# Kernel optimization log

Measured on AMD Instinct MI355X. Metric: run time of the kernel, lower is better.

Reference implementation:

```python
import jax, jax.numpy as jnp
import numpy as np

# irreps '32x0e + 32x1o + 16x2e': dims 32 (l=0), 96 (l=1, 32x3), 80 (l=2, 16x5) -> 208
MUL0, MUL1, MUL2 = 32, 32, 16
SC = 64  # scalar_channels
N_NODES, N_EDGES = 50000, 200000
FAN_IN = MUL0 * MUL0 + MUL1 * MUL1 + MUL2 * MUL2  # fully-connected path fan-in


def setup_inputs() -> dict:
    key = jax.random.key(0)
    ks = jax.random.split(key, 10)
    node_tensors = jax.random.normal(ks[0], (N_NODES, 208), dtype=jnp.float32)
    edge_index = jax.random.randint(ks[1], (2, N_EDGES), 0, N_NODES)
    # FullyConnectedTensorProduct path weights (mul1, mul2, mul_out)
    W0 = jax.random.normal(ks[2], (MUL0, MUL0, SC), dtype=jnp.float32)
    W1 = jax.random.normal(ks[3], (MUL1, MUL1, SC), dtype=jnp.float32)
    W2 = jax.random.normal(ks[4], (MUL2, MUL2, SC), dtype=jnp.float32)
    # MLP: Linear(64,32) -> SiLU -> Linear(32,1)
    A1 = jax.random.normal(ks[5], (SC, SC // 2), dtype=jnp.float32) / np.float32(np.sqrt(SC))
    b1 = jnp.zeros((SC // 2,), dtype=jnp.float32)
    A2 = jax.random.normal(ks[6], (SC // 2, 1), dtype=jnp.float32) / np.float32(np.sqrt(SC // 2))
    b2 = jnp.zeros((1,), dtype=jnp.float32)
    return {"node_tensors": node_tensors, "edge_index": edge_index,
            "W0": W0, "W1": W1, "W2": W2, "A1": A1, "b1": b1, "A2": A2, "b2": b2}


def _split_irreps(x):
    # x: [E, 208] -> scalars [E,32], vectors [E,32,3], rank-2 [E,16,5]
    s = x[:, :MUL0]
    v = x[:, MUL0:MUL0 + MUL1 * 3].reshape(-1, MUL1, 3)
    t = x[:, MUL0 + MUL1 * 3:].reshape(-1, MUL2, 5)
    return s, v, t


def reference(node_tensors, edge_index, W0, W1, W2, A1, b1, A2, b2):
    src, dst = edge_index[0], edge_index[1]
    x1 = node_tensors[src]  # [E, 208]
    x2 = node_tensors[dst]
    s1, v1, t1 = _split_irreps(x1)
    s2, v2, t2 = _split_irreps(x2)
    alpha = np.float32(1.0 / np.sqrt(FAN_IN))  # path normalization
    # l x l -> 0 Clebsch-Gordan: delta_{m1 m2} / sqrt(2l+1)
    e = alpha * (
        jnp.einsum('eu,ev,uvw->ew', s1, s2, W0)
        + jnp.einsum('eum,evm,uvw->ew', v1, v2, W1) / np.float32(np.sqrt(3.0))
        + jnp.einsum('eum,evm,uvw->ew', t1, t2, W2) / np.float32(np.sqrt(5.0))
    )  # [E, 64]
    h = jax.nn.silu(e @ A1 + b1)
    return (h @ A2 + b2)[:, 0]  # [E]
```

## Files before the change

### kernel.cpp

```cpp
#include <hip/hip_runtime.h>
#include <hip/hip_fp16.h>
#include <stdint.h>

#define N_EDGES 200000
#define N_NODES 50000
#define BM 256
#define NT 512

typedef _Float16 f16x8 __attribute__((ext_vector_type(8)));
typedef float f32x4 __attribute__((ext_vector_type(4)));

__global__ void prep_w(const float* __restrict__ W0, const float* __restrict__ W1,
                       const float* __restrict__ W2, uint16_t* __restrict__ wt) {
  int o = blockIdx.x * 256 + threadIdx.x;
  int T = o >> 11, r = o & 2047, w = r >> 5, kk = r & 31;
  int k = T * 32 + kk;
  const float AS = 1.0f / 48.0f;
  const float AV = AS * 0.57735026918962576f;
  const float AT = AS * 0.44721359549995794f;
  float val;
  if (k < 1024)      val = AS * W0[(k >> 5) * 2048 + (k & 31) * 64 + w];
  else if (k < 2048) { int k2 = k - 1024; val = AV * W1[(k2 >> 5) * 2048 + (k2 & 31) * 64 + w]; }
  else               { int k2 = k - 2048; val = AT * W2[(k2 >> 4) * 1024 + (k2 & 15) * 64 + w]; }
  __half h = __float2half(val);
  wt[o] = *reinterpret_cast<uint16_t*>(&h);
}

__global__ void prep_tables(const float* __restrict__ nt,
                            uint16_t* __restrict__ ta, uint16_t* __restrict__ tb) {
  long long o = (long long)blockIdx.x * 256 + threadIdx.x;
  if (o >= (long long)N_NODES * 296) return;
  int node = (int)(o / 296);
  int r = (int)(o - (long long)node * 296);
  const float* x = nt + (size_t)node * 208;
  float va = 0.f;
  if (r < 32) va = x[r];
  else if (r < 160) { int q = r - 32;  int u = q >> 2, m = q & 3;  if (m < 3) va = x[32 + u * 3 + m]; }
  else if (r < 288) { int q = r - 160; int u = q >> 3, m = q & 7;  if (m < 5) va = x[128 + u * 5 + m]; }
  __half ha = __float2half(va);
  ta[(size_t)node * 296 + r] = *reinterpret_cast<uint16_t*>(&ha);
  if (r < 216) {
    float vb = 0.f;
    if (r < 32) vb = x[r];
    else if (r < 128) { int q = r - 32;  int m = q >> 5, v = q & 31; vb = x[32 + v * 3 + m]; }
    else if (r < 208) { int q = r - 128; int m = q >> 4, v = q & 15; vb = x[128 + v * 5 + m]; }
    __half hb = __float2half(vb);
    tb[(size_t)node * 216 + r] = *reinterpret_cast<uint16_t*>(&hb);
  }
}

__device__ __forceinline__ void gload16(const void* g, void* l) {
  __builtin_amdgcn_global_load_lds(
      (const __attribute__((address_space(1))) void*)g,
      (__attribute__((address_space(3))) void*)l, 16, 0, 0);
}

#define LOADW(WRA, TEXPR)                                                       \
  { int Tc_ = (TEXPR);                                                          \
    _Pragma("unroll") for (int nf = 0; nf < 4; ++nf)                            \
      WRA[nf] = wtg4[Tc_ * 256 + nf * 64 + lo4]; }

#define MSTEP4(WRA, A)                                                          \
  _Pragma("unroll") for (int mf = 0; mf < 4; ++mf)                              \
  _Pragma("unroll") for (int nf = 0; nf < 4; ++nf)                              \
    acc[mf][nf] = __builtin_amdgcn_mfma_f32_16x16x32_f16(                       \
        (A)[mf], *(const f16x8*)&WRA[nf], acc[mf][nf], 0, 0, 0);

#define MSTEP2(WRA, A, H)                                                       \
  _Pragma("unroll") for (int mm = 0; mm < 2; ++mm)                              \
  _Pragma("unroll") for (int nf = 0; nf < 4; ++nf)                              \
    acc[2 * (H) + mm][nf] = __builtin_amdgcn_mfma_f32_16x16x32_f16(             \
        (A)[mm], *(const f16x8*)&WRA[nf], acc[2 * (H) + mm][nf], 0, 0, 0);

#define BUILD_S(T_, A)                                                          \
  _Pragma("unroll") for (int mf = 0; mf < 4; ++mf) {                            \
    __half s1v = *(const __half*)(x1b[mf] + 2 * (T_));                          \
    __half2 s1b2 = __half2half2(s1v);                                           \
    union { uint32_t u[4]; f16x8 v; } au_;                                      \
    _Pragma("unroll") for (int q = 0; q < 4; ++q) {                             \
      __half2 p = __hmul2(s1b2, ((const __half2*)&s2pk[mf])[q]);                \
      au_.u[q] = *(uint32_t*)&p;                                                \
    }                                                                           \
    (A)[mf] = au_.v;                                                            \
  }

#define BUILD_V(U_, A)                                                          \
  _Pragma("unroll") for (int mf = 0; mf < 4; ++mf) {                            \
    uint2 vv_ = *(const uint2*)(x1b[mf] + 64 + (U_) * 8);                       \
    __half2 h01_ = *(__half2*)&vv_.x;                                           \
    __half2 h2x_ = *(__half2*)&vv_.y;                                           \
    __half2 va0 = __half2half2(__low2half(h01_));                               \
    __half2 va1 = __half2half2(__high2half(h01_));                              \
    __half2 va2 = __half2half2(__low2half(h2x_));                               \
    union { uint32_t u[4]; f16x8 v; } au_;                                      \
    _Pragma("unroll") for (int q = 0; q < 4; ++q) {                             \
      __half2 p = __hmul2(va0, ((const __half2*)&v2pk[mf][0])[q]);              \
      p = __hfma2(va1, ((const __half2*)&v2pk[mf][1])[q], p);                   \
      p = __hfma2(va2, ((const __half2*)&v2pk[mf][2])[q], p);                   \
      au_.u[q] = *(uint32_t*)&p;                                                \
    }                                                                           \
    (A)[mf] = au_.v;                                                            \
  }

#define BUILD_TH(TT_, H, A)                                                     \
  _Pragma("unroll") for (int mm = 0; mm < 2; ++mm) {                            \
    int u_ = (TT_) * 2 + (g >> 1);                                              \
    uint4 tv_ = *(const uint4*)(x1b[2 * (H) + mm] + 320 + u_ * 16);             \
    __half2 w01_ = *(__half2*)&tv_.x;                                           \
    __half2 w23_ = *(__half2*)&tv_.y;                                           \
    __half2 w4x_ = *(__half2*)&tv_.z;                                           \
    __half2 tb0 = __half2half2(__low2half(w01_));                               \
    __half2 tb1 = __half2half2(__high2half(w01_));                              \
    __half2 tb2 = __half2half2(__low2half(w23_));                               \
    __half2 tb3 = __half2half2(__high2half(w23_));                              \
    __half2 tb4 = __half2half2(__low2half(w4x_));                               \
    union { uint32_t u[4]; f16x8 v; } au_;                                      \
    _Pragma("unroll") for (int q = 0; q < 4; ++q) {                             \
      __half2 p = __hmul2(tb0, ((const __half2*)&t2pk[mm][0])[q]);              \
      p = __hfma2(tb1, ((const __half2*)&t2pk[mm][1])[q], p);                   \
      p = __hfma2(tb2, ((const __half2*)&t2pk[mm][2])[q], p);                   \
      p = __hfma2(tb3, ((const __half2*)&t2pk[mm][3])[q], p);                   \
      p = __hfma2(tb4, ((const __half2*)&t2pk[mm][4])[q], p);                   \
      au_.u[q] = *(uint32_t*)&p;                                                \
    }                                                                           \
    (A)[mm] = au_.v;                                                            \
  }

#define RING_S(WRA, P, T0) { f16x8 a[4]; BUILD_S((T0) + (P), a); MSTEP4(WRA, a); LOADW(WRA, (T0) + (P) + 4); }
#define RING_V(WRA, P, T0) { f16x8 a[4]; BUILD_V((T0) + (P) - 32, a); MSTEP4(WRA, a); LOADW(WRA, (T0) + (P) + 4); }
#define WRAPT(X) ((X) <= 71 ? (X) : (X) - 8)
#define RING_T(WRA, P, T0, H) { f16x8 a[2]; BUILD_TH((T0) + (P) - 64, H, a); MSTEP2(WRA, a, H); LOADW(WRA, WRAPT((T0) + (P) + 4)); }

__global__ __launch_bounds__(NT, 2) void edge_main(
    const uint16_t* __restrict__ ta, const uint16_t* __restrict__ tbl,
    const int* __restrict__ ei, const uint16_t* __restrict__ wt,
    const float* __restrict__ A1, const float* __restrict__ b1,
    const float* __restrict__ A2, const float* __restrict__ b2,
    float* __restrict__ out)
{
  __shared__ alignas(16) unsigned char smem[151552];
  const int tid = threadIdx.x;
  const int e0 = blockIdx.x * BM;

  {
    #pragma unroll
    for (int i = 0; i < 18; ++i) {
      unsigned idx = i * 512 + tid;
      unsigned row = idx / 37u;
      unsigned cj = idx - row * 37u;
      int e = e0 + (int)row; if (e > N_EDGES - 1) e = N_EDGES - 1;
      int src = ei[e];
      const char* gp = (const char*)ta + (size_t)src * 592 + cj * 16;
      void* lp = (void*)(smem + i * 8192 + (tid >> 6) * 1024);
      gload16(gp, lp);
    }
    if (tid < 256) {
      unsigned idx = 9216 + tid;
      unsigned row = idx / 37u;
      unsigned cj = idx - row * 37u;
      int e = e0 + (int)row; if (e > N_EDGES - 1) e = N_EDGES - 1;
      int src = ei[e];
      const char* gp = (const char*)ta + (size_t)src * 592 + cj * 16;
      void* lp = (void*)(smem + 147456 + (tid >> 6) * 1024);
      gload16(gp, lp);
    }
  }
  asm volatile("s_waitcnt vmcnt(0)" ::: "memory");
  __syncthreads();

  const int lane = tid & 63, c = lane & 15, g = lane >> 4;
  const int wv = tid >> 6;
  const int m = wv >> 1;
  const int kh = wv & 1;
  const int lo4 = c * 4 + g;

  const unsigned char* x1b[4];
  const unsigned char* tbp[4];
  #pragma unroll
  for (int mf = 0; mf < 4; ++mf) {
    int erow = m * 64 + mf * 16 + c;
    x1b[mf] = smem + (size_t)erow * 592;
    int e = e0 + erow; if (e > N_EDGES - 1) e = N_EDGES - 1;
    int dst = ei[N_EDGES + e];
    tbp[mf] = (const unsigned char*)tbl + (size_t)dst * 432;
  }

  f32x4 acc[4][4];
  #pragma unroll
  for (int mf = 0; mf < 4; ++mf)
    #pragma unroll
    for (int nf = 0; nf < 4; ++nf) acc[mf][nf] = (f32x4){0.f, 0.f, 0.f, 0.f};

  const uint4* wtg4 = (const uint4*)wt;
  uint4 wr0[4], wr1[4], wr2[4], wr3[4];

  if (kh == 0) {
    uint4 s2pk[4];
    #pragma unroll
    for (int mf = 0; mf < 4; ++mf) s2pk[mf] = *(const uint4*)(tbp[mf] + g * 16);
    LOADW(wr0, 0); LOADW(wr1, 1); LOADW(wr2, 2); LOADW(wr3, 3);
    for (int T = 0; T < 32; T += 4) {
      RING_S(wr0, 0, T); RING_S(wr1, 1, T); RING_S(wr2, 2, T); RING_S(wr3, 3, T);
    }
    uint4 v2pk[4][3];
    #pragma unroll
    for (int mf = 0; mf < 4; ++mf)
      #pragma unroll
      for (int m3 = 0; m3 < 3; ++m3)
        v2pk[mf][m3] = *(const uint4*)(tbp[mf] + 64 + m3 * 64 + g * 16);
    for (int T = 32; T < 44; T += 4) {
      RING_V(wr0, 0, T); RING_V(wr1, 1, T); RING_V(wr2, 2, T); RING_V(wr3, 3, T);
    }
  } else {
    uint4 v2pk[4][3];
    #pragma unroll
    for (int mf = 0; mf < 4; ++mf)
      #pragma unroll
      for (int m3 = 0; m3 < 3; ++m3)
        v2pk[mf][m3] = *(const uint4*)(tbp[mf] + 64 + m3 * 64 + g * 16);
    LOADW(wr0, 44); LOADW(wr1, 45); LOADW(wr2, 46); LOADW(wr3, 47);
    for (int T = 44; T < 64; T += 4) {
      RING_V(wr0, 0, T); RING_V(wr1, 1, T); RING_V(wr2, 2, T); RING_V(wr3, 3, T);
    }
    {
      uint4 t2pk[2][5];
      #pragma unroll
      for (int mm = 0; mm < 2; ++mm)
        #pragma unroll
        for (int m5 = 0; m5 < 5; ++m5)
          t2pk[mm][m5] = *(const uint4*)(tbp[mm] + 256 + m5 * 32 + (g & 1) * 16);
      RING_T(wr0, 0, 64, 0); RING_T(wr1, 1, 64, 0); RING_T(wr2, 2, 64, 0); RING_T(wr3, 3, 64, 0);
      RING_T(wr0, 0, 68, 0); RING_T(wr1, 1, 68, 0); RING_T(wr2, 2, 68, 0); RING_T(wr3, 3, 68, 0);
    }
    {
      uint4 t2pk[2][5];
      #pragma unroll
      for (int mm = 0; mm < 2; ++mm)
        #pragma unroll
        for (int m5 = 0; m5 < 5; ++m5)
          t2pk[mm][m5] = *(const uint4*)(tbp[2 + mm] + 256 + m5 * 32 + (g & 1) * 16);
      RING_T(wr0, 0, 64, 1); RING_T(wr1, 1, 64, 1); RING_T(wr2, 2, 64, 1); RING_T(wr3, 3, 64, 1);
      RING_T(wr0, 0, 68, 1); RING_T(wr1, 1, 68, 1); RING_T(wr2, 2, 68, 1); RING_T(wr3, 3, 68, 1);
    }
  }

  __syncthreads();
  float* etile = (float*)smem;
  #pragma unroll
  for (int mf = 0; mf < 4; ++mf)
    #pragma unroll
    for (int nf = 0; nf < 4; ++nf)
      #pragma unroll
      for (int rr = 0; rr < 4; ++rr)
        etile[(size_t)(kh * 256 + m * 64 + mf * 16 + g * 4 + rr) * 68 + nf * 16 + c] =
            acc[mf][nf][rr];
  {
    float4* d4 = (float4*)(smem + 139264);
    d4[tid] = ((const float4*)A1)[tid];
  }
  __syncthreads();

  {
    int el = tid >> 1, jh = tid & 1;
    const float* er0 = etile + (size_t)el * 68;
    const float* er1 = etile + (size_t)(256 + el) * 68;
    const float* A1s = (const float*)(smem + 139264);
    float hacc[16];
    #pragma unroll
    for (int j = 0; j < 16; ++j) hacc[j] = b1[jh * 16 + j];
    for (int w4 = 0; w4 < 16; ++w4) {
      float4 ea = *(const float4*)(er0 + w4 * 4);
      float4 eb = *(const float4*)(er1 + w4 * 4);
      #pragma unroll
      for (int q2 = 0; q2 < 4; ++q2) {
        float ev = (&ea.x)[q2] + (&eb.x)[q2];
        int w = w4 * 4 + q2;
        float4 a0 = *(const float4*)(A1s + w * 32 + jh * 16);
        float4 a1 = *(const float4*)(A1s + w * 32 + jh * 16 + 4);
        float4 a2 = *(const float4*)(A1s + w * 32 + jh * 16 + 8);
        float4 a3 = *(const float4*)(A1s + w * 32 + jh * 16 + 12);
        hacc[0]  += ev * a0.x; hacc[1]  += ev * a0.y; hacc[2]  += ev * a0.z; hacc[3]  += ev * a0.w;
        hacc[4]  += ev * a1.x; hacc[5]  += ev * a1.y; hacc[6]  += ev * a1.z; hacc[7]  += ev * a1.w;
        hacc[8]  += ev * a2.x; hacc[9]  += ev * a2.y; hacc[10] += ev * a2.z; hacc[11] += ev * a2.w;
        hacc[12] += ev * a3.x; hacc[13] += ev * a3.y; hacc[14] += ev * a3.z; hacc[15] += ev * a3.w;
      }
    }
    float o = 0.f;
    #pragma unroll
    for (int j = 0; j < 16; ++j) {
      float z = hacc[j];
      o += (z / (1.f + __expf(-z))) * A2[jh * 16 + j];
    }
    o += __shfl_xor(o, 1);
    int e = e0 + el;
    if (jh == 0 && e < N_EDGES) out[e] = o + b2[0];
  }
}

extern "C" void kernel_launch(void* const* d_in, const int* in_sizes, int n_in,
                              void* d_out, int out_size, void* d_ws, size_t ws_size,
                              hipStream_t stream) {
  const float* nt = (const float*)d_in[0];
  const int*   ei = (const int*)d_in[1];
  const float* W0 = (const float*)d_in[2];
  const float* W1 = (const float*)d_in[3];
  const float* W2 = (const float*)d_in[4];
  const float* A1 = (const float*)d_in[5];
  const float* b1 = (const float*)d_in[6];
  const float* A2 = (const float*)d_in[7];
  const float* b2 = (const float*)d_in[8];
  float* out = (float*)d_out;

  uint16_t* wt = (uint16_t*)d_ws;
  uint16_t* ta = (uint16_t*)((char*)d_ws + 294912);
  uint16_t* tb = (uint16_t*)((char*)d_ws + 294912 + (size_t)N_NODES * 592);

  prep_w<<<576, 256, 0, stream>>>(W0, W1, W2, wt);
  {
    long long tot = (long long)N_NODES * 296;
    int blocks = (int)((tot + 255) / 256);
    prep_tables<<<blocks, 256, 0, stream>>>(nt, ta, tb);
  }
  edge_main<<<(N_EDGES + BM - 1) / BM, NT, 0, stream>>>(ta, tb, ei, wt, A1, b1, A2, b2, out);
}
```

Measured before the change: 184.7 us.

## Halve edge tile to 128 rows per block to raise occupancy

Measured after the change: 255.7 us. 1.38x slower.

```diff
diff --git a/kernel.cpp b/kernel.cpp
--- a/kernel.cpp
+++ b/kernel.cpp
@@ -4,7 +4,7 @@
 
 #define N_EDGES 200000
 #define N_NODES 50000
-#define BM 256
+#define BM 128
 #define NT 512
 
 typedef _Float16 f16x8 __attribute__((ext_vector_type(8)));
@@ -60,20 +60,14 @@
     _Pragma("unroll") for (int nf = 0; nf < 4; ++nf)                            \
       WRA[nf] = wtg4[Tc_ * 256 + nf * 64 + lo4]; }
 
-#define MSTEP4(WRA, A)                                                          \
-  _Pragma("unroll") for (int mf = 0; mf < 4; ++mf)                              \
+#define MSTEPA(WRA, A)                                                          \
+  _Pragma("unroll") for (int mf = 0; mf < 2; ++mf)                              \
   _Pragma("unroll") for (int nf = 0; nf < 4; ++nf)                              \
     acc[mf][nf] = __builtin_amdgcn_mfma_f32_16x16x32_f16(                       \
         (A)[mf], *(const f16x8*)&WRA[nf], acc[mf][nf], 0, 0, 0);
 
-#define MSTEP2(WRA, A, H)                                                       \
-  _Pragma("unroll") for (int mm = 0; mm < 2; ++mm)                              \
-  _Pragma("unroll") for (int nf = 0; nf < 4; ++nf)                              \
-    acc[2 * (H) + mm][nf] = __builtin_amdgcn_mfma_f32_16x16x32_f16(             \
-        (A)[mm], *(const f16x8*)&WRA[nf], acc[2 * (H) + mm][nf], 0, 0, 0);
-
 #define BUILD_S(T_, A)                                                          \
-  _Pragma("unroll") for (int mf = 0; mf < 4; ++mf) {                            \
+  _Pragma("unroll") for (int mf = 0; mf < 2; ++mf) {                            \
     __half s1v = *(const __half*)(x1b[mf] + 2 * (T_));                          \
     __half2 s1b2 = __half2half2(s1v);                                           \
     union { uint32_t u[4]; f16x8 v; } au_;                                      \
@@ -85,7 +79,7 @@
   }
 
 #define BUILD_V(U_, A)                                                          \
-  _Pragma("unroll") for (int mf = 0; mf < 4; ++mf) {                            \
+  _Pragma("unroll") for (int mf = 0; mf < 2; ++mf) {                            \
     uint2 vv_ = *(const uint2*)(x1b[mf] + 64 + (U_) * 8);                       \
     __half2 h01_ = *(__half2*)&vv_.x;                                           \
     __half2 h2x_ = *(__half2*)&vv_.y;                                           \
@@ -102,10 +96,10 @@
     (A)[mf] = au_.v;                                                            \
   }
 
-#define BUILD_TH(TT_, H, A)                                                     \
+#define BUILD_T(TT_, A)                                                         \
   _Pragma("unroll") for (int mm = 0; mm < 2; ++mm) {                            \
     int u_ = (TT_) * 2 + (g >> 1);                                              \
-    uint4 tv_ = *(const uint4*)(x1b[2 * (H) + mm] + 320 + u_ * 16);             \
+    uint4 tv_ = *(const uint4*)(x1b[mm] + 320 + u_ * 16);                       \
     __half2 w01_ = *(__half2*)&tv_.x;                                           \
     __half2 w23_ = *(__half2*)&tv_.y;                                           \
     __half2 w4x_ = *(__half2*)&tv_.z;                                           \
@@ -126,25 +120,25 @@
     (A)[mm] = au_.v;                                                            \
   }
 
-#define RING_S(WRA, P, T0) { f16x8 a[4]; BUILD_S((T0) + (P), a); MSTEP4(WRA, a); LOADW(WRA, (T0) + (P) + 4); }
-#define RING_V(WRA, P, T0) { f16x8 a[4]; BUILD_V((T0) + (P) - 32, a); MSTEP4(WRA, a); LOADW(WRA, (T0) + (P) + 4); }
+#define RING_S(WRA, P, T0) { f16x8 a[2]; BUILD_S((T0) + (P), a); MSTEPA(WRA, a); LOADW(WRA, (T0) + (P) + 4); }
+#define RING_V(WRA, P, T0) { f16x8 a[2]; BUILD_V((T0) + (P) - 32, a); MSTEPA(WRA, a); LOADW(WRA, (T0) + (P) + 4); }
 #define WRAPT(X) ((X) <= 71 ? (X) : (X) - 8)
-#define RING_T(WRA, P, T0, H) { f16x8 a[2]; BUILD_TH((T0) + (P) - 64, H, a); MSTEP2(WRA, a, H); LOADW(WRA, WRAPT((T0) + (P) + 4)); }
-
-__global__ __launch_bounds__(NT, 2) void edge_main(
+#define RING_T(WRA, P, T0) { f16x8 a[2]; BUILD_T((T0) + (P) - 64, a); MSTEPA(WRA, a); LOADW(WRA, WRAPT((T0) + (P) + 4)); }
+
+__global__ __launch_bounds__(NT, 4) void edge_main(
     const uint16_t* __restrict__ ta, const uint16_t* __restrict__ tbl,
     const int* __restrict__ ei, const uint16_t* __restrict__ wt,
     const float* __restrict__ A1, const float* __restrict__ b1,
     const float* __restrict__ A2, const float* __restrict__ b2,
     float* __restrict__ out)
 {
-  __shared__ alignas(16) unsigned char smem[151552];
+  __shared__ alignas(16) unsigned char smem[77824];
   const int tid = threadIdx.x;
   const int e0 = blockIdx.x * BM;
 
   {
     #pragma unroll
-    for (int i = 0; i < 18; ++i) {
+    for (int i = 0; i < 9; ++i) {
       unsigned idx = i * 512 + tid;
       unsigned row = idx / 37u;
       unsigned cj = idx - row * 37u;
@@ -154,14 +148,14 @@
       void* lp = (void*)(smem + i * 8192 + (tid >> 6) * 1024);
       gload16(gp, lp);
     }
-    if (tid < 256) {
-      unsigned idx = 9216 + tid;
+    if (tid < 128) {
+      unsigned idx = 4608 + tid;
       unsigned row = idx / 37u;
       unsigned cj = idx - row * 37u;
       int e = e0 + (int)row; if (e > N_EDGES - 1) e = N_EDGES - 1;
       int src = ei[e];
       const char* gp = (const char*)ta + (size_t)src * 592 + cj * 16;
-      void* lp = (void*)(smem + 147456 + (tid >> 6) * 1024);
+      void* lp = (void*)(smem + 73728 + (tid >> 6) * 1024);
       gload16(gp, lp);
     }
   }
@@ -174,20 +168,20 @@
   const int kh = wv & 1;
   const int lo4 = c * 4 + g;
 
-  const unsigned char* x1b[4];
-  const unsigned char* tbp[4];
+  const unsigned char* x1b[2];
+  const unsigned char* tbp[2];
   #pragma unroll
-  for (int mf = 0; mf < 4; ++mf) {
-    int erow = m * 64 + mf * 16 + c;
+  for (int mf = 0; mf < 2; ++mf) {
+    int erow = m * 32 + mf * 16 + c;
     x1b[mf] = smem + (size_t)erow * 592;
     int e = e0 + erow; if (e > N_EDGES - 1) e = N_EDGES - 1;
     int dst = ei[N_EDGES + e];
     tbp[mf] = (const unsigned char*)tbl + (size_t)dst * 432;
   }
 
-  f32x4 acc[4][4];
+  f32x4 acc[2][4];
   #pragma unroll
-  for (int mf = 0; mf < 4; ++mf)
+  for (int mf = 0; mf < 2; ++mf)
     #pragma unroll
     for (int nf = 0; nf < 4; ++nf) acc[mf][nf] = (f32x4){0.f, 0.f, 0.f, 0.f};
 
@@ -195,16 +189,16 @@
   uint4 wr0[4], wr1[4], wr2[4], wr3[4];
 
   if (kh == 0) {
-    uint4 s2pk[4];
-    #pragma unroll
-    for (int mf = 0; mf < 4; ++mf) s2pk[mf] = *(const uint4*)(tbp[mf] + g * 16);
+    uint4 s2pk[2];
+    #pragma unroll
+    for (int mf = 0; mf < 2; ++mf) s2pk[mf] = *(const uint4*)(tbp[mf] + g * 16);
     LOADW(wr0, 0); LOADW(wr1, 1); LOADW(wr2, 2); LOADW(wr3, 3);
     for (int T = 0; T < 32; T += 4) {
       RING_S(wr0, 0, T); RING_S(wr1, 1, T); RING_S(wr2, 2, T); RING_S(wr3, 3, T);
     }
-    uint4 v2pk[4][3];
-    #pragma unroll
-    for (int mf = 0; mf < 4; ++mf)
+    uint4 v2pk[2][3];
+    #pragma unroll
+    for (int mf = 0; mf < 2; ++mf)
       #pragma unroll
       for (int m3 = 0; m3 < 3; ++m3)
         v2pk[mf][m3] = *(const uint4*)(tbp[mf] + 64 + m3 * 64 + g * 16);
@@ -212,9 +206,9 @@
       RING_V(wr0, 0, T); RING_V(wr1, 1, T); RING_V(wr2, 2, T); RING_V(wr3, 3, T);
     }
   } else {
-    uint4 v2pk[4][3];
-    #pragma unroll
-    for (int mf = 0; mf < 4; ++mf)
+    uint4 v2pk[2][3];
+    #pragma unroll
+    for (int mf = 0; mf < 2; ++mf)
       #pragma unroll
       for (int m3 = 0; m3 < 3; ++m3)
         v2pk[mf][m3] = *(const uint4*)(tbp[mf] + 64 + m3 * 64 + g * 16);
@@ -229,42 +223,32 @@
         #pragma unroll
         for (int m5 = 0; m5 < 5; ++m5)
           t2pk[mm][m5] = *(const uint4*)(tbp[mm] + 256 + m5 * 32 + (g & 1) * 16);
-      RING_T(wr0, 0, 64, 0); RING_T(wr1, 1, 64, 0); RING_T(wr2, 2, 64, 0); RING_T(wr3, 3, 64, 0);
-      RING_T(wr0, 0, 68, 0); RING_T(wr1, 1, 68, 0); RING_T(wr2, 2, 68, 0); RING_T(wr3, 3, 68, 0);
-    }
-    {
-      uint4 t2pk[2][5];
-      #pragma unroll
-      for (int mm = 0; mm < 2; ++mm)
-        #pragma unroll
-        for (int m5 = 0; m5 < 5; ++m5)
-          t2pk[mm][m5] = *(const uint4*)(tbp[2 + mm] + 256 + m5 * 32 + (g & 1) * 16);
-      RING_T(wr0, 0, 64, 1); RING_T(wr1, 1, 64, 1); RING_T(wr2, 2, 64, 1); RING_T(wr3, 3, 64, 1);
-      RING_T(wr0, 0, 68, 1); RING_T(wr1, 1, 68, 1); RING_T(wr2, 2, 68, 1); RING_T(wr3, 3, 68, 1);
+      RING_T(wr0, 0, 64); RING_T(wr1, 1, 64); RING_T(wr2, 2, 64); RING_T(wr3, 3, 64);
+      RING_T(wr0, 0, 68); RING_T(wr1, 1, 68); RING_T(wr2, 2, 68); RING_T(wr3, 3, 68);
     }
   }
 
   __syncthreads();
   float* etile = (float*)smem;
   #pragma unroll
-  for (int mf = 0; mf < 4; ++mf)
+  for (int mf = 0; mf < 2; ++mf)
     #pragma unroll
     for (int nf = 0; nf < 4; ++nf)
       #pragma unroll
       for (int rr = 0; rr < 4; ++rr)
-        etile[(size_t)(kh * 256 + m * 64 + mf * 16 + g * 4 + rr) * 68 + nf * 16 + c] =
+        etile[(size_t)(kh * 128 + m * 32 + mf * 16 + g * 4 + rr) * 68 + nf * 16 + c] =
             acc[mf][nf][rr];
   {
-    float4* d4 = (float4*)(smem + 139264);
+    float4* d4 = (float4*)(smem + 69632);
     d4[tid] = ((const float4*)A1)[tid];
   }
   __syncthreads();
 
-  {
+  if (tid < 256) {
     int el = tid >> 1, jh = tid & 1;
     const float* er0 = etile + (size_t)el * 68;
-    const float* er1 = etile + (size_t)(256 + el) * 68;
-    const float* A1s = (const float*)(smem + 139264);
+    const float* er1 = etile + (size_t)(128 + el) * 68;
+    const float* A1s = (const float*)(smem + 69632);
     float hacc[16];
     #pragma unroll
     for (int j = 0; j < 16; ++j) hacc[j] = b1[jh * 16 + j];
```
